# Kernel optimization log

Hardware: AMD Instinct MI355X
Metric: run time of the kernel (lower is better)

The kernel has to match this reference:

```python
import jax, jax.numpy as jnp
import numpy as np

B, N, HW, PS, FHW = 16, 4096, 224, 8, 56

def _gelu(x):
    return jax.nn.gelu(x, approximate=True)  # tanh approximation, matches nn.GELU(approximate='tanh')

def _conv(x, w, b, stride):
    y = jax.lax.conv_general_dilated(x, w, (stride, stride), [(1, 1), (1, 1)],
                                     dimension_numbers=('NCHW', 'OIHW', 'NCHW'))
    return y + b[None, :, None, None]

def _embed(points):
    # for i in 0..11: append sin(2^i * p) then cos(2^i * p) -> [B,N,48]
    factors = 2.0 ** jnp.arange(12, dtype=points.dtype)
    scaled = points[..., None, :] * factors[:, None]          # [B,N,12,2]
    feats = jnp.concatenate([jnp.sin(scaled), jnp.cos(scaled)], axis=-1)  # [B,N,12,4]
    return feats.reshape(points.shape[0], points.shape[1], 48)

def _extract_patches(fmap, points):
    # fmap [B,C,H,W]; points in [0,1]; bilinear grid_sample, zeros padding, align_corners=True
    Bq, C, H, W = fmap.shape
    centers = points * 2.0 - 1.0
    step = 2.0 / (W - 1)
    half = (PS - 1) / 2.0
    offs = jnp.linspace(-half, half, PS, dtype=fmap.dtype) * step
    offx2d, offy2d = jnp.meshgrid(offs, offs, indexing='ij')   # [ps,ps]
    gx = centers[..., 0][..., None, None] + offx2d             # [B,N,ps,ps]
    gy = centers[..., 1][..., None, None] + offy2d
    # align_corners=True pixel coords
    ix = (gx + 1.0) * 0.5 * (W - 1)
    iy = (gy + 1.0) * 0.5 * (H - 1)
    x0f = jnp.floor(ix); y0f = jnp.floor(iy)
    x0 = x0f.astype(jnp.int32); y0 = y0f.astype(jnp.int32)
    x1 = x0 + 1; y1 = y0 + 1
    wx1 = ix - x0f; wx0 = 1.0 - wx1
    wy1 = iy - y0f; wy0 = 1.0 - wy1
    fflat = fmap.reshape(Bq, C, H * W)

    def corner(xi, yi, w):
        valid = ((xi >= 0) & (xi < W) & (yi >= 0) & (yi < H)).astype(fmap.dtype)
        idx = jnp.clip(yi, 0, H - 1) * W + jnp.clip(xi, 0, W - 1)   # [B,N,ps,ps]
        vals = jax.vmap(lambda f, i: f[:, i])(fflat, idx)           # [B,C,N,ps,ps]
        return vals * (w * valid)[:, None]

    out = (corner(x0, y0, wx0 * wy0) + corner(x1, y0, wx1 * wy0)
           + corner(x0, y1, wx0 * wy1) + corner(x1, y1, wx1 * wy1))  # [B,C,N,ps,ps]
    return out.transpose(0, 2, 1, 3, 4)                              # [B,N,C,ps,ps]

def setup_inputs():
    key = jax.random.key(0)
    ks = jax.random.split(key, 26)
    def w(k, shape):
        fan_in = int(np.prod(shape[1:]))
        return jax.random.normal(k, shape, jnp.float32) * (1.0 / np.sqrt(fan_in))
    inp = {
        'points': jax.random.uniform(ks[0], (B, N, 2), jnp.float32),
        'images': jax.random.normal(ks[1], (B, 3, HW, HW), jnp.float32),
        # plane encoder
        'pw1': w(ks[2], (16, 3, 3, 3)),  'pb1': jnp.zeros((16,), jnp.float32),
        'pw2': w(ks[3], (32, 16, 3, 3)), 'pb2': jnp.zeros((32,), jnp.float32),
        'pw3': w(ks[4], (4, 32, 3, 3)),  'pb3': jnp.zeros((4,), jnp.float32),
        # global encoder
        'gw1': w(ks[5], (4, 3, 3, 3)),   'gb1': jnp.zeros((4,), jnp.float32),
        'gw2': w(ks[6], (8, 4, 3, 3)),   'gb2': jnp.zeros((8,), jnp.float32),
        'gw3': w(ks[7], (16, 8, 3, 3)),  'gb3': jnp.zeros((16,), jnp.float32),
        'gw4': w(ks[8], (32, 16, 3, 3)), 'gb4': jnp.zeros((32,), jnp.float32),
        'gw5': w(ks[9], (64, 32, 3, 3)), 'gb5': jnp.zeros((64,), jnp.float32),
        # point encoder (torch Linear: [out,in])
        'lw1': w(ks[10], (256, 48)),  'lb1': jnp.zeros((256,), jnp.float32),
        'lw2': w(ks[11], (256, 256)), 'lb2': jnp.zeros((256,), jnp.float32),
        # head
        'hw1': w(ks[12], (512, 576)), 'hb1': jnp.zeros((512,), jnp.float32),
        'hw2': w(ks[13], (1, 512)),   'hb2': jnp.zeros((1,), jnp.float32),
    }
    return inp

def reference(points, images, pw1, pb1, pw2, pb2, pw3, pb3,
              gw1, gb1, gw2, gb2, gw3, gb3, gw4, gb4, gw5, gb5,
              lw1, lb1, lw2, lb2, hw1, hb1, hw2, hb2):
    # point branch
    pe = _embed(points)                                         # [B,N,48]
    pf = _gelu(pe @ lw1.T + lb1) @ lw2.T + lb2                  # [B,N,256]
    # plane encoder -> 4x56x56 fmap
    f = _gelu(_conv(images, pw1, pb1, 2))
    f = _gelu(_conv(f, pw2, pb2, 2))
    fmap = _gelu(_conv(f, pw3, pb3, 1))                         # [B,4,56,56]
    # global encoder -> [B,64]
    g = images
    for wg, bg in ((gw1, gb1), (gw2, gb2), (gw3, gb3), (gw4, gb4), (gw5, gb5)):
        g = _gelu(_conv(g, wg, bg, 2))
    gc = g.mean(axis=(2, 3))                                    # AvgPool2d(7)+Flatten -> [B,64]
    gc = jnp.broadcast_to(gc[:, None, :], (points.shape[0], points.shape[1], 64))
    # per-point bilinear patch gather
    patches = _extract_patches(fmap, points).reshape(points.shape[0], points.shape[1], -1)  # [B,N,256]
    fused = jnp.concatenate([pf, patches, gc], axis=-1)         # [B,N,576]
    logit = _gelu(fused @ hw1.T + hb1) @ hw2.T + hb2            # [B,N,1]
    return logit
```

## Files before the change

### kernel.cpp

```cpp
#include <hip/hip_runtime.h>
#include <math.h>

#define BB 16
#define NN 4096
#define M_TOT (BB*NN)
#define TBK 32

typedef __attribute__((ext_vector_type(8))) short s8v;
typedef __attribute__((ext_vector_type(4))) float f4v;

__device__ __forceinline__ float gelu_t(float x){
    float u = 1.5957691216057308f * x * (1.0f + 0.044715f*x*x);
    return x / (1.0f + __expf(-u));
}

__device__ __forceinline__ unsigned short f2bf(float f){
    unsigned int u = __float_as_uint(f);
    u += 0x7fffu + ((u >> 16) & 1u);
    return (unsigned short)(u >> 16);
}

#define GLL(src, dst) __builtin_amdgcn_global_load_lds( \
    (const __attribute__((address_space(1))) void*)(src), \
    (__attribute__((address_space(3))) void*)(dst), 16, 0, 0)

template<int CIN, int COUT, int STRIDE, int CHUNK>
__device__ __forceinline__ void conv_dev2(
    const float* __restrict__ in, const float* __restrict__ w,
    const float* __restrict__ bias, float* __restrict__ out,
    int Hin, int Win, int Hout, int Wout, int bx, int by, int b, float* tile)
{
    constexpr int IW = 15*STRIDE + 3;
    constexpr int IH = IW;
    constexpr int PITCH = IW + 1;
    int tid = threadIdx.x;
    int tx = tid & 15, ty = tid >> 4;
    int wo = bx*16 + tx;
    int ho = by*16 + ty;
    int win0 = bx*16*STRIDE - 1;
    int hin0 = by*16*STRIDE - 1;
    bool valid = (wo < Wout) && (ho < Hout);

    float acc[COUT];
    #pragma unroll
    for (int co = 0; co < COUT; ++co) acc[co] = bias[co];

    const float* ib = in + (size_t)(b*CIN)*Hin*Win;
    for (int ci0 = 0; ci0 < CIN; ci0 += CHUNK) {
        __syncthreads();
        for (int idx = tid; idx < CHUNK*IH*IW; idx += 256) {
            int c = idx / (IH*IW), rem = idx - c*(IH*IW);
            int r = rem / IW, cc = rem - r*IW;
            int hi = hin0 + r, wi = win0 + cc;
            float v = 0.f;
            if ((unsigned)hi < (unsigned)Hin && (unsigned)wi < (unsigned)Win)
                v = ib[(size_t)(ci0 + c)*Hin*Win + hi*Win + wi];
            tile[c*IH*PITCH + r*PITCH + cc] = v;
        }
        __syncthreads();
        for (int ci = 0; ci < CHUNK; ++ci) {
            float vv[9];
            const float* tb = tile + ci*IH*PITCH;
            #pragma unroll
            for (int kh = 0; kh < 3; ++kh)
                #pragma unroll
                for (int kw = 0; kw < 3; ++kw)
                    vv[kh*3+kw] = tb[(ty*STRIDE + kh)*PITCH + tx*STRIDE + kw];
            const float* wc = w + (ci0 + ci)*9;
            #pragma unroll
            for (int co = 0; co < COUT; ++co) {
                const float* wp = wc + co*CIN*9;
                #pragma unroll
                for (int k = 0; k < 9; ++k)
                    acc[co] = fmaf(vv[k], wp[k], acc[co]);
            }
        }
    }
    if (valid) {
        size_t obase = ((size_t)b*COUT)*Hout*Wout + (size_t)ho*Wout + wo;
        #pragma unroll
        for (int co = 0; co < COUT; ++co)
            out[obase + (size_t)co*Hout*Wout] = gelu_t(acc[co]);
    }
}

__device__ __forceinline__ void conv_p3_dev(
    const float* __restrict__ in, const float* __restrict__ w,
    const float* __restrict__ bias, float4* __restrict__ out,
    int bx, int by, int b, float* tile)
{
    int tid = threadIdx.x;
    int tx = tid & 15, ty = tid >> 4;
    int wo = bx*16 + tx;
    int ho = by*16 + ty;
    int win0 = bx*16 - 1;
    int hin0 = by*16 - 1;
    bool valid = (ho < 56) && (wo < 56);

    const float* ib = in + (size_t)(b*32)*3136;
    __syncthreads();
    for (int idx = tid; idx < 32*324; idx += 256) {
        int c = idx / 324, rem = idx - c*324;
        int r = rem / 18, cc = rem - r*18;
        int hi = hin0 + r, wi = win0 + cc;
        float v = 0.f;
        if ((unsigned)hi < 56u && (unsigned)wi < 56u)
            v = ib[(size_t)c*3136 + hi*56 + wi];
        tile[c*342 + r*19 + cc] = v;
    }
    __syncthreads();
    float acc[4];
    #pragma unroll
    for (int co = 0; co < 4; ++co) acc[co] = bias[co];
    for (int ci = 0; ci < 32; ++ci) {
        float vv[9];
        const float* tb = tile + ci*342;
        #pragma unroll
        for (int kh = 0; kh < 3; ++kh)
            #pragma unroll
            for (int kw = 0; kw < 3; ++kw)
                vv[kh*3+kw] = tb[(ty + kh)*19 + tx + kw];
        #pragma unroll
        for (int co = 0; co < 4; ++co) {
            const float* wp = w + co*288 + ci*9;
            #pragma unroll
            for (int k = 0; k < 9; ++k)
                acc[co] = fmaf(vv[k], wp[k], acc[co]);
        }
    }
    if (valid) {
        float4 o;
        o.x = gelu_t(acc[0]); o.y = gelu_t(acc[1]);
        o.z = gelu_t(acc[2]); o.w = gelu_t(acc[3]);
        out[(size_t)b*3136 + (size_t)ho*56 + wo] = o;
    }
}

__global__ __launch_bounds__(256) void conv_dual_k(
    const float* __restrict__ in,
    const float* __restrict__ wA, const float* __restrict__ bA,
    const float* __restrict__ wB, const float* __restrict__ bB,
    float* __restrict__ outA, float* __restrict__ outB)
{
    __shared__ float tile[3*33*34];
    const int Hin = 224, Win = 224, Hout = 112, Wout = 112;
    int tid = threadIdx.x;
    int tx = tid & 15, ty = tid >> 4;
    int b = blockIdx.z;
    int wo = blockIdx.x*16 + tx;
    int ho = blockIdx.y*16 + ty;
    int win0 = blockIdx.x*32 - 1;
    int hin0 = blockIdx.y*32 - 1;

    const float* ib = in + (size_t)(b*3)*Hin*Win;
    for (int idx = tid; idx < 3*1089; idx += 256) {
        int c = idx / 1089, rem = idx - c*1089;
        int r = rem / 33, cc = rem - r*33;
        int hi = hin0 + r, wi = win0 + cc;
        float v = 0.f;
        if ((unsigned)hi < (unsigned)Hin && (unsigned)wi < (unsigned)Win)
            v = ib[(size_t)c*Hin*Win + hi*Win + wi];
        tile[c*33*34 + r*34 + cc] = v;
    }
    __syncthreads();

    float accA[16], accB[4];
    #pragma unroll
    for (int co = 0; co < 16; ++co) accA[co] = bA[co];
    #pragma unroll
    for (int co = 0; co < 4; ++co) accB[co] = bB[co];

    #pragma unroll
    for (int ci = 0; ci < 3; ++ci) {
        float vv[9];
        const float* tb = tile + ci*33*34;
        #pragma unroll
        for (int kh = 0; kh < 3; ++kh)
            #pragma unroll
            for (int kw = 0; kw < 3; ++kw)
                vv[kh*3+kw] = tb[(ty*2 + kh)*34 + tx*2 + kw];
        #pragma unroll
        for (int co = 0; co < 16; ++co) {
            const float* wp = wA + co*27 + ci*9;
            #pragma unroll
            for (int k = 0; k < 9; ++k) accA[co] = fmaf(vv[k], wp[k], accA[co]);
        }
        #pragma unroll
        for (int co = 0; co < 4; ++co) {
            const float* wp = wB + co*27 + ci*9;
            #pragma unroll
            for (int k = 0; k < 9; ++k) accB[co] = fmaf(vv[k], wp[k], accB[co]);
        }
    }
    size_t px = (size_t)ho*Wout + wo;
    #pragma unroll
    for (int co = 0; co < 16; ++co)
        outA[((size_t)(b*16 + co))*Hout*Wout + px] = gelu_t(accA[co]);
    #pragma unroll
    for (int co = 0; co < 4; ++co)
        outB[((size_t)(b*4 + co))*Hout*Wout + px] = gelu_t(accB[co]);
}

__global__ __launch_bounds__(256) void conv_pg2_k(
    const float* __restrict__ f1, const float* __restrict__ pw2, const float* __restrict__ pb2, float* __restrict__ f2,
    const float* __restrict__ g1, const float* __restrict__ gw2, const float* __restrict__ gb2, float* __restrict__ g2)
{
    __shared__ float tile[8*33*34];
    int z = blockIdx.z;
    if (z < 16) conv_dev2<16,32,2,8>(f1, pw2, pb2, f2, 112,112, 56,56, blockIdx.x, blockIdx.y, z, tile);
    else        conv_dev2<4,8,2,4> (g1, gw2, gb2, g2, 112,112, 56,56, blockIdx.x, blockIdx.y, z-16, tile);
}

__global__ __launch_bounds__(256) void conv_pg3_k(
    const float* __restrict__ f2, const float* __restrict__ pw3, const float* __restrict__ pb3, float4* __restrict__ fmap4,
    const float* __restrict__ g2, const float* __restrict__ gw3, const float* __restrict__ gb3, float* __restrict__ g3)
{
    __shared__ float tile[32*342];
    int z = blockIdx.z;
    if (z < 16) {
        conv_p3_dev(f2, pw3, pb3, fmap4, blockIdx.x, blockIdx.y, z, tile);
    } else {
        if (blockIdx.x >= 2 || blockIdx.y >= 2) return;
        conv_dev2<8,16,2,8>(g2, gw3, gb3, g3, 56,56, 28,28, blockIdx.x, blockIdx.y, z-16, tile);
    }
}

__global__ __launch_bounds__(256) void g4_k(
    const float* __restrict__ g3, const float* __restrict__ w4,
    const float* __restrict__ b4, float* __restrict__ g4)
{
    __shared__ float ws[32*144];
    int tid = threadIdx.x;
    for (int i = tid; i < 32*144; i += 256) ws[i] = w4[i];
    __syncthreads();
    int idx = blockIdx.x*256 + tid;
    if (idx >= 16*196) return;
    int b = idx / 196, px = idx - (idx/196)*196;
    int ho = px / 14, wo = px - (px/14)*14;
    const float* src = g3 + (size_t)b*16*784;
    float acc[32];
    #pragma unroll
    for (int co = 0; co < 32; ++co) acc[co] = b4[co];
    for (int ci = 0; ci < 16; ++ci) {
        #pragma unroll
        for (int kh = 0; kh < 3; ++kh) {
            int hi = ho*2 - 1 + kh;
            if ((unsigned)hi >= 28u) continue;
            #pragma unroll
            for (int kw = 0; kw < 3; ++kw) {
                int wi = wo*2 - 1 + kw;
                if ((unsigned)wi >= 28u) continue;
                float v = src[ci*784 + hi*28 + wi];
                int wofs = ci*9 + kh*3 + kw;
                #pragma unroll
                for (int co = 0; co < 32; ++co)
                    acc[co] = fmaf(v, ws[co*144 + wofs], acc[co]);
            }
        }
    }
    size_t obase = (size_t)b*32*196 + px;
    #pragma unroll
    for (int co = 0; co < 32; ++co)
        g4[obase + (size_t)co*196] = gelu_t(acc[co]);
}

__global__ __launch_bounds__(256) void g5_k(
    const float* __restrict__ g4, const float* __restrict__ w5,
    const float* __restrict__ b5, float* __restrict__ g5)
{
    __shared__ float ws[64*288];
    int tid = threadIdx.x;
    for (int i = tid; i < 64*288; i += 256) ws[i] = w5[i];
    __syncthreads();
    int idx = blockIdx.x*256 + tid;
    if (idx >= 16*49*2) return;
    int cg = idx & 1;
    int t = idx >> 1;
    int b = t / 49, px = t - (t/49)*49;
    int ho = px / 7, wo = px - (px/7)*7;
    const float* src = g4 + (size_t)b*32*196;
    const float* wsb = ws + cg*32*288;
    float acc[32];
    #pragma unroll
    for (int c = 0; c < 32; ++c) acc[c] = b5[cg*32 + c];
    for (int ci = 0; ci < 32; ++ci) {
        #pragma unroll
        for (int kh = 0; kh < 3; ++kh) {
            int hi = ho*2 - 1 + kh;
            if ((unsigned)hi >= 14u) continue;
            #pragma unroll
            for (int kw = 0; kw < 3; ++kw) {
                int wi = wo*2 - 1 + kw;
                if ((unsigned)wi >= 14u) continue;
                float v = src[ci*196 + hi*14 + wi];
                int wofs = ci*9 + kh*3 + kw;
                #pragma unroll
                for (int c = 0; c < 32; ++c)
                    acc[c] = fmaf(v, wsb[c*288 + wofs], acc[c]);
            }
        }
    }
    size_t obase = (size_t)b*64*49 + (size_t)cg*32*49 + px;
    #pragma unroll
    for (int c = 0; c < 32; ++c)
        g5[obase + (size_t)c*49] = gelu_t(acc[c]);
}

__global__ void avgpool7_k(const float* __restrict__ in, float* __restrict__ out){
    int i = blockIdx.x*blockDim.x + threadIdx.x;
    if (i >= BB*64) return;
    const float* p = in + (size_t)i*49;
    float s = 0.f;
    #pragma unroll
    for (int k = 0; k < 49; ++k) s += p[k];
    out[i] = s * (1.0f/49.0f);
}

__global__ void cvtall_k(const float* __restrict__ lw1, const float* __restrict__ lw2,
                         const float* __restrict__ hw1, unsigned short* __restrict__ blw1,
                         unsigned short* __restrict__ blw2, unsigned short* __restrict__ bhw1,
                         float* __restrict__ out, const float* __restrict__ b2){
    int i = blockIdx.x*blockDim.x + threadIdx.x;
    if (i < M_TOT) out[i] = b2[0];
    if (i < 256*64) {
        int r = i >> 6, c = i & 63;
        blw1[i] = (c < 48) ? f2bf(lw1[r*48 + c]) : 0;
        return;
    }
    int j = i - 256*64;
    if (j < 256*256) { blw2[j] = f2bf(lw2[j]); return; }
    j -= 256*256;
    if (j < 512*576) bhw1[j] = f2bf(hw1[j]);
}

__global__ __launch_bounds__(512) void mlp12_k(
    const float* __restrict__ points,
    const unsigned short* __restrict__ W1, const float* __restrict__ b1,
    const unsigned short* __restrict__ W2, const float* __restrict__ b2,
    unsigned short* __restrict__ C,
    const float4* __restrict__ fmap4, const float* __restrict__ gc)
{
    __shared__ unsigned short Hd[128*256];
    __shared__ unsigned short B2[256*TBK];
    int tid = threadIdx.x;
    int wv = tid >> 6, lane = tid & 63;
    int q = lane >> 4, lr = lane & 15;
    int mi = wv >> 2, ni = wv & 3;
    size_t m0 = (size_t)blockIdx.x * 128;

    f4v acc1[4][4];
    #pragma unroll
    for (int i = 0; i < 4; ++i)
        #pragma unroll
        for (int j = 0; j < 4; ++j) acc1[i][j] = (f4v){0.f,0.f,0.f,0.f};

    #pragma unroll
    for (int kb = 0; kb < 2; ++kb) {
        int seg = kb*4 + q;
        s8v a[4], b[4];
        #pragma unroll
        for (int t = 0; t < 4; ++t) {
            size_t m = m0 + mi*64 + t*16 + lr;
            float px = points[m*2], py = points[m*2+1];
            union { s8v v; unsigned short u[8]; } pk;
            #pragma unroll
            for (int j = 0; j < 8; ++j) {
                int k = seg*8 + j;
                unsigned short val = 0;
                if (k < 48) {
                    int i2 = k >> 2, rr = k & 3;
                    float f = (float)(1 << i2);
                    float p = (rr & 1) ? py : px;
                    float s = f * p;
                    val = f2bf((rr < 2) ? __sinf(s) : __cosf(s));
                }
                pk.u[j] = val;
            }
            a[t] = pk.v;
        }
        #pragma unroll
        for (int t = 0; t < 4; ++t) {
            int n = ni*64 + t*16 + lr;
            b[t] = *(const s8v*)(W1 + n*64 + seg*8);
        }
        #pragma unroll
        for (int mt = 0; mt < 4; ++mt)
            #pragma unroll
            for (int nt = 0; nt < 4; ++nt)
                acc1[mt][nt] = __builtin_amdgcn_mfma_f32_16x16x32_bf16(a[mt], b[nt], acc1[mt][nt], 0, 0, 0);
    }
    {
        float b1v[4];
        #pragma unroll
        for (int nt = 0; nt < 4; ++nt) b1v[nt] = b1[ni*64 + nt*16 + lr];
        #pragma unroll
        for (int mt = 0; mt < 4; ++mt)
            #pragma unroll
            for (int r4 = 0; r4 < 4; ++r4) {
                int row = mi*64 + mt*16 + q*4 + r4;
                #pragma unroll
                for (int nt = 0; nt < 4; ++nt) {
                    int col = ni*64 + nt*16 + lr;
                    float v = gelu_t(acc1[mt][nt][r4] + b1v[nt]);
                    int p = (col >> 3) ^ (row & 7);
                    Hd[(row*32 + p)*8 + (col & 7)] = f2bf(v);
                }
            }
    }
    __syncthreads();

    f4v acc2[4][4];
    #pragma unroll
    for (int i = 0; i < 4; ++i)
        #pragma unroll
        for (int j = 0; j < 4; ++j) acc2[i][j] = (f4v){0.f,0.f,0.f,0.f};

    for (int kt = 0; kt < 8; ++kt) {
        #pragma unroll
        for (int r = 0; r < 2; ++r) {
            int f = r*512 + tid;
            int rr = f >> 2, ll = (f & 3) ^ ((f >> 3) & 3);
            GLL(W2 + rr*256 + kt*32 + ll*8, B2 + f*8);
        }
        __syncthreads();
        s8v a[4], b[4];
        int sw = q ^ ((lr >> 1) & 3);
        #pragma unroll
        for (int t = 0; t < 4; ++t) {
            int row = mi*64 + t*16 + lr;
            int p = (kt*4 + q) ^ (row & 7);
            a[t] = *(const s8v*)(Hd + (row*32 + p)*8);
        }
        #pragma unroll
        for (int t = 0; t < 4; ++t) {
            int n = ni*64 + t*16 + lr;
            b[t] = *(const s8v*)(B2 + (n*4 + sw)*8);
        }
        #pragma unroll
        for (int mt = 0; mt < 4; ++mt)
            #pragma unroll
            for (int nt = 0; nt < 4; ++nt)
                acc2[mt][nt] = __builtin_amdgcn_mfma_f32_16x16x32_bf16(a[mt], b[nt], acc2[mt][nt], 0, 0, 0);
        __syncthreads();
    }
    {
        float b2v[4];
        #pragma unroll
        for (int nt = 0; nt < 4; ++nt) b2v[nt] = b2[ni*64 + nt*16 + lr];
        #pragma unroll
        for (int mt = 0; mt < 4; ++mt)
            #pragma unroll
            for (int r4 = 0; r4 < 4; ++r4) {
                size_t m = m0 + mi*64 + mt*16 + q*4 + r4;
                #pragma unroll
                for (int nt = 0; nt < 4; ++nt) {
                    int n = ni*64 + nt*16 + lr;
                    C[m*576 + n] = f2bf(acc2[mt][nt][r4] + b2v[nt]);
                }
            }
    }
    #pragma unroll 1
    for (int it = 0; it < 16; ++it) {
        int task = it*512 + tid;
        int ml = task >> 6, ij = task & 63;
        size_t m = m0 + ml;
        int i = ij >> 3, j = ij & 7;
        int b = (int)(m >> 12);
        float px = points[m*2], py = points[m*2+1];
        float cx = px*2.f - 1.f, cy = py*2.f - 1.f;
        const float step = 2.0f/55.0f;
        float gx = cx + ((float)i - 3.5f)*step;
        float gy = cy + ((float)j - 3.5f)*step;
        float ix = (gx + 1.f)*0.5f*55.f;
        float iy = (gy + 1.f)*0.5f*55.f;
        float x0f = floorf(ix), y0f = floorf(iy);
        int x0 = (int)x0f, y0 = (int)y0f;
        int x1 = x0 + 1,  y1 = y0 + 1;
        float wx1 = ix - x0f, wx0 = 1.f - wx1;
        float wy1 = iy - y0f, wy0 = 1.f - wy1;
        float v00 = ((x0>=0)&&(x0<56)&&(y0>=0)&&(y0<56)) ? 1.f : 0.f;
        float v10 = ((x1>=0)&&(x1<56)&&(y0>=0)&&(y0<56)) ? 1.f : 0.f;
        float v01 = ((x0>=0)&&(x0<56)&&(y1>=0)&&(y1<56)) ? 1.f : 0.f;
        float v11 = ((x1>=0)&&(x1<56)&&(y1>=0)&&(y1<56)) ? 1.f : 0.f;
        float w00 = wx0*wy0*v00, w10 = wx1*wy0*v10, w01 = wx0*wy1*v01, w11 = wx1*wy1*v11;
        int cx0 = min(max(x0,0),55), cx1 = min(max(x1,0),55);
        int cy0 = min(max(y0,0),55), cy1 = min(max(y1,0),55);
        const float4* fb = fmap4 + (size_t)b*3136;
        float4 f00 = fb[cy0*56 + cx0], f10 = fb[cy0*56 + cx1];
        float4 f01 = fb[cy1*56 + cx0], f11 = fb[cy1*56 + cx1];
        float4 v;
        v.x = w00*f00.x + w10*f10.x + w01*f01.x + w11*f11.x;
        v.y = w00*f00.y + w10*f10.y + w01*f01.y + w11*f11.y;
        v.z = w00*f00.z + w10*f10.z + w01*f01.z + w11*f11.z;
        v.w = w00*f00.w + w10*f10.w + w01*f01.w + w11*f11.w;
        C[m*576 + 256 +   0 + ij] = f2bf(v.x);
        C[m*576 + 256 +  64 + ij] = f2bf(v.y);
        C[m*576 + 256 + 128 + ij] = f2bf(v.z);
        C[m*576 + 256 + 192 + ij] = f2bf(v.w);
        C[m*576 + 512 + ij] = f2bf(gc[b*64 + ij]);
    }
}

__global__ __launch_bounds__(256, 3) void gemm_hd_k(
    const unsigned short* __restrict__ A,
    const unsigned short* __restrict__ W,
    const float* __restrict__ bias, const float* __restrict__ w2,
    float* __restrict__ out)
{
    __shared__ unsigned short As[64*TBK];
    __shared__ unsigned short Bs[256*TBK];
    __shared__ float red[4*64];
    int tid = threadIdx.x;
    int wv = tid >> 6, lane = tid & 63;
    int q = lane >> 4, lr = lane & 15;
    int sw = q ^ ((lr >> 1) & 3);
    int nq = wv * 64;
    size_t m0 = (size_t)blockIdx.x * 64;
    int nbase = blockIdx.y * 256;

    int rA = tid >> 2;
    int lA = (tid & 3) ^ ((tid >> 3) & 3);
    const unsigned short* srcA = A + (m0 + rA)*576 + lA*8;
    unsigned short* dstA = As + tid*8;
    const unsigned short* srcB[4]; unsigned short* dstB[4];
    #pragma unroll
    for (int r = 0; r < 4; ++r) {
        int f = r*256 + tid;
        int rr = f >> 2, ll = (f & 3) ^ ((f >> 3) & 3);
        srcB[r] = W + (size_t)(nbase + rr)*576 + ll*8;
        dstB[r] = Bs + f*8;
    }

    f4v acc[4][4];
    #pragma unroll
    for (int i = 0; i < 4; ++i)
        #pragma unroll
        for (int j = 0; j < 4; ++j) acc[i][j] = (f4v){0.f,0.f,0.f,0.f};

    for (int k0 = 0; k0 < 576; k0 += TBK) {
        GLL(srcA, dstA); srcA += TBK;
        #pragma unroll
        for (int r = 0; r < 4; ++r) { GLL(srcB[r], dstB[r]); srcB[r] += TBK; }
        __syncthreads();
        s8v a[4], b[4];
        #pragma unroll
        for (int t = 0; t < 4; ++t)
            a[t] = *(const s8v*)(As + (t*16 + lr)*TBK + sw*8);
        #pragma unroll
        for (int t = 0; t < 4; ++t)
            b[t] = *(const s8v*)(Bs + (nq + t*16 + lr)*TBK + sw*8);
        #pragma unroll
        for (int mt = 0; mt < 4; ++mt)
            #pragma unroll
            for (int nt = 0; nt < 4; ++nt)
                acc[mt][nt] = __builtin_amdgcn_mfma_f32_16x16x32_bf16(a[mt], b[nt], acc[mt][nt], 0, 0, 0);
        __syncthreads();
    }
    float bv[4], w2v[4];
    #pragma unroll
    for (int nt = 0; nt < 4; ++nt) {
        int n = nbase + nq + nt*16 + lr;
        bv[nt] = bias[n];
        w2v[nt] = w2[n];
    }
    #pragma unroll
    for (int mt = 0; mt < 4; ++mt)
        #pragma unroll
        for (int r4 = 0; r4 < 4; ++r4) {
            int ml = mt*16 + q*4 + r4;
            float s = 0.f;
            #pragma unroll
            for (int nt = 0; nt < 4; ++nt)
                s += gelu_t(acc[mt][nt][r4] + bv[nt]) * w2v[nt];
            #pragma unroll
            for (int off = 8; off > 0; off >>= 1) s += __shfl_down(s, off, 16);
            if (lr == 0) red[wv*64 + ml] = s;
        }
    __syncthreads();
    if (tid < 64) {
        float t = red[tid] + red[64 + tid] + red[128 + tid] + red[192 + tid];
        atomicAdd(&out[m0 + tid], t);
    }
}

extern "C" void kernel_launch(void* const* d_in, const int* in_sizes, int n_in,
                              void* d_out, int out_size, void* d_ws, size_t ws_size,
                              hipStream_t stream) {
    const float* points = (const float*)d_in[0];
    const float* images = (const float*)d_in[1];
    const float* pw1 = (const float*)d_in[2];  const float* pb1 = (const float*)d_in[3];
    const float* pw2 = (const float*)d_in[4];  const float* pb2 = (const float*)d_in[5];
    const float* pw3 = (const float*)d_in[6];  const float* pb3 = (const float*)d_in[7];
    const float* gw1 = (const float*)d_in[8];  const float* gb1 = (const float*)d_in[9];
    const float* gw2 = (const float*)d_in[10]; const float* gb2 = (const float*)d_in[11];
    const float* gw3 = (const float*)d_in[12]; const float* gb3 = (const float*)d_in[13];
    const float* gw4 = (const float*)d_in[14]; const float* gb4 = (const float*)d_in[15];
    const float* gw5 = (const float*)d_in[16]; const float* gb5 = (const float*)d_in[17];
    const float* lw1 = (const float*)d_in[18]; const float* lb1 = (const float*)d_in[19];
    const float* lw2 = (const float*)d_in[20]; const float* lb2 = (const float*)d_in[21];
    const float* hw1 = (const float*)d_in[22]; const float* hb1 = (const float*)d_in[23];
    const float* hw2 = (const float*)d_in[24]; const float* hb2 = (const float*)d_in[25];
    float* out = (float*)d_out;

    char* base = (char*)d_ws;
    unsigned short* fused_b = (unsigned short*)base;
    unsigned short* hid_b   = fused_b + (size_t)M_TOT*576;
    float4* fmap4 = (float4*)(hid_b + (size_t)M_TOT*256);
    float* gc   = (float*)(fmap4 + (size_t)16*3136);
    unsigned short* blw1 = (unsigned short*)(gc + 1024);
    unsigned short* blw2 = blw1 + 256*64;
    unsigned short* bhw1 = blw2 + 256*256;
    float* ct = (float*)base;
    float* f1 = ct;
    float* f2 = f1 + (size_t)16*16*112*112;
    float* g1 = f2 + (size_t)16*32*56*56;
    float* g2 = g1 + (size_t)16*4*112*112;
    float* g3 = g2 + (size_t)16*8*56*56;
    float* g4 = g3 + (size_t)16*16*28*28;
    float* g5 = g4 + (size_t)16*32*14*14;

    cvtall_k<<<1472, 256, 0, stream>>>(lw1, lw2, hw1, blw1, blw2, bhw1, out, hb2);
    conv_dual_k<<<dim3(7,7,16), 256, 0, stream>>>(images, pw1, pb1, gw1, gb1, f1, g1);
    conv_pg2_k<<<dim3(4,4,32), 256, 0, stream>>>(f1, pw2, pb2, f2, g1, gw2, gb2, g2);
    conv_pg3_k<<<dim3(4,4,32), 256, 0, stream>>>(f2, pw3, pb3, fmap4, g2, gw3, gb3, g3);
    g4_k<<<13, 256, 0, stream>>>(g3, gw4, gb4, g4);
    g5_k<<<7, 256, 0, stream>>>(g4, gw5, gb5, g5);
    avgpool7_k<<<4, 256, 0, stream>>>(g5, gc);
    mlp12_k<<<M_TOT/128, 512, 0, stream>>>(points, blw1, lb1, blw2, lb2, fused_b, fmap4, gc);
    gemm_hd_k<<<dim3(M_TOT/64, 2), 256, 0, stream>>>(fused_b, bhw1, hb1, hw2, out);
}
```

Baseline: 489.7 us.

## Widen parallelism of small global-encoder convs and fuse avgpool via atomics

Splits the plane conv2 over two output-channel halves to double block count, and rewrites the plane conv3 to read directly from global memory with one thread per pixel, dropping the large shared tile. The g4 and g5 convs now assign one output channel per thread with an NHWC intermediate, so they launch many more blocks. The avgpool kernel is removed: g5 atomically accumulates the pooled mean into gc, which cvtall zeroes first. The aim is to stop the tiny tail convs from running on a handful of blocks, at the cost of more redundant global loads and nondeterministic float summation order.

```diff
diff --git a/kernel.cpp b/kernel.cpp
--- a/kernel.cpp
+++ b/kernel.cpp
@@ -84,58 +84,6 @@
     }
 }
 
-__device__ __forceinline__ void conv_p3_dev(
-    const float* __restrict__ in, const float* __restrict__ w,
-    const float* __restrict__ bias, float4* __restrict__ out,
-    int bx, int by, int b, float* tile)
-{
-    int tid = threadIdx.x;
-    int tx = tid & 15, ty = tid >> 4;
-    int wo = bx*16 + tx;
-    int ho = by*16 + ty;
-    int win0 = bx*16 - 1;
-    int hin0 = by*16 - 1;
-    bool valid = (ho < 56) && (wo < 56);
-
-    const float* ib = in + (size_t)(b*32)*3136;
-    __syncthreads();
-    for (int idx = tid; idx < 32*324; idx += 256) {
-        int c = idx / 324, rem = idx - c*324;
-        int r = rem / 18, cc = rem - r*18;
-        int hi = hin0 + r, wi = win0 + cc;
-        float v = 0.f;
-        if ((unsigned)hi < 56u && (unsigned)wi < 56u)
-            v = ib[(size_t)c*3136 + hi*56 + wi];
-        tile[c*342 + r*19 + cc] = v;
-    }
-    __syncthreads();
-    float acc[4];
-    #pragma unroll
-    for (int co = 0; co < 4; ++co) acc[co] = bias[co];
-    for (int ci = 0; ci < 32; ++ci) {
-        float vv[9];
-        const float* tb = tile + ci*342;
-        #pragma unroll
-        for (int kh = 0; kh < 3; ++kh)
-            #pragma unroll
-            for (int kw = 0; kw < 3; ++kw)
-                vv[kh*3+kw] = tb[(ty + kh)*19 + tx + kw];
-        #pragma unroll
-        for (int co = 0; co < 4; ++co) {
-            const float* wp = w + co*288 + ci*9;
-            #pragma unroll
-            for (int k = 0; k < 9; ++k)
-                acc[co] = fmaf(vv[k], wp[k], acc[co]);
-        }
-    }
-    if (valid) {
-        float4 o;
-        o.x = gelu_t(acc[0]); o.y = gelu_t(acc[1]);
-        o.z = gelu_t(acc[2]); o.w = gelu_t(acc[3]);
-        out[(size_t)b*3136 + (size_t)ho*56 + wo] = o;
-    }
-}
-
 __global__ __launch_bounds__(256) void conv_dual_k(
     const float* __restrict__ in,
     const float* __restrict__ wA, const float* __restrict__ bA,
@@ -207,40 +155,72 @@
 {
     __shared__ float tile[8*33*34];
     int z = blockIdx.z;
-    if (z < 16) conv_dev2<16,32,2,8>(f1, pw2, pb2, f2, 112,112, 56,56, blockIdx.x, blockIdx.y, z, tile);
-    else        conv_dev2<4,8,2,4> (g1, gw2, gb2, g2, 112,112, 56,56, blockIdx.x, blockIdx.y, z-16, tile);
+    if (z < 32) {
+        int b = z >> 1, half = z & 1;
+        conv_dev2<16,16,2,8>(f1 + (size_t)b*16*12544, pw2 + half*2304, pb2 + half*16,
+                             f2 + ((size_t)(b*32 + half*16))*3136,
+                             112,112, 56,56, blockIdx.x, blockIdx.y, 0, tile);
+    } else {
+        conv_dev2<4,8,2,4>(g1, gw2, gb2, g2, 112,112, 56,56, blockIdx.x, blockIdx.y, z-32, tile);
+    }
 }
 
 __global__ __launch_bounds__(256) void conv_pg3_k(
     const float* __restrict__ f2, const float* __restrict__ pw3, const float* __restrict__ pb3, float4* __restrict__ fmap4,
     const float* __restrict__ g2, const float* __restrict__ gw3, const float* __restrict__ gb3, float* __restrict__ g3)
 {
-    __shared__ float tile[32*342];
+    __shared__ float tile[8*33*34];
     int z = blockIdx.z;
     if (z < 16) {
-        conv_p3_dev(f2, pw3, pb3, fmap4, blockIdx.x, blockIdx.y, z, tile);
+        int b = z;
+        int idx = blockIdx.x*256 + threadIdx.x;
+        if (idx >= 3136) return;
+        int ho = idx / 56, wo = idx - ho*56;
+        const float* ib = f2 + (size_t)b*32*3136;
+        float acc[4];
+        #pragma unroll
+        for (int co = 0; co < 4; ++co) acc[co] = pb3[co];
+        for (int ci = 0; ci < 32; ++ci) {
+            const float* ic = ib + (size_t)ci*3136;
+            #pragma unroll
+            for (int kh = 0; kh < 3; ++kh) {
+                int hi = ho - 1 + kh;
+                if ((unsigned)hi >= 56u) continue;
+                #pragma unroll
+                for (int kw = 0; kw < 3; ++kw) {
+                    int wi = wo - 1 + kw;
+                    if ((unsigned)wi >= 56u) continue;
+                    float v = ic[hi*56 + wi];
+                    int wofs = ci*9 + kh*3 + kw;
+                    #pragma unroll
+                    for (int co = 0; co < 4; ++co)
+                        acc[co] = fmaf(v, pw3[co*288 + wofs], acc[co]);
+                }
+            }
+        }
+        float4 o;
+        o.x = gelu_t(acc[0]); o.y = gelu_t(acc[1]);
+        o.z = gelu_t(acc[2]); o.w = gelu_t(acc[3]);
+        fmap4[(size_t)b*3136 + idx] = o;
     } else {
-        if (blockIdx.x >= 2 || blockIdx.y >= 2) return;
-        conv_dev2<8,16,2,8>(g2, gw3, gb3, g3, 56,56, 28,28, blockIdx.x, blockIdx.y, z-16, tile);
+        if (blockIdx.x >= 4) return;
+        int bx = blockIdx.x & 1, by = blockIdx.x >> 1;
+        conv_dev2<8,16,2,8>(g2, gw3, gb3, g3, 56,56, 28,28, bx, by, z-16, tile);
     }
 }
 
 __global__ __launch_bounds__(256) void g4_k(
     const float* __restrict__ g3, const float* __restrict__ w4,
-    const float* __restrict__ b4, float* __restrict__ g4)
-{
-    __shared__ float ws[32*144];
-    int tid = threadIdx.x;
-    for (int i = tid; i < 32*144; i += 256) ws[i] = w4[i];
-    __syncthreads();
-    int idx = blockIdx.x*256 + tid;
-    if (idx >= 16*196) return;
-    int b = idx / 196, px = idx - (idx/196)*196;
-    int ho = px / 14, wo = px - (px/14)*14;
+    const float* __restrict__ b4, float* __restrict__ g4o)
+{
+    int idx = blockIdx.x*256 + threadIdx.x;
+    int co = idx & 31;
+    int t = idx >> 5;
+    int b = t / 196, px = t - b*196;
+    int ho = px / 14, wo = px - ho*14;
     const float* src = g3 + (size_t)b*16*784;
-    float acc[32];
-    #pragma unroll
-    for (int co = 0; co < 32; ++co) acc[co] = b4[co];
+    const float* wp = w4 + co*144;
+    float acc = b4[co];
     for (int ci = 0; ci < 16; ++ci) {
         #pragma unroll
         for (int kh = 0; kh < 3; ++kh) {
@@ -250,39 +230,25 @@
             for (int kw = 0; kw < 3; ++kw) {
                 int wi = wo*2 - 1 + kw;
                 if ((unsigned)wi >= 28u) continue;
-                float v = src[ci*784 + hi*28 + wi];
-                int wofs = ci*9 + kh*3 + kw;
-                #pragma unroll
-                for (int co = 0; co < 32; ++co)
-                    acc[co] = fmaf(v, ws[co*144 + wofs], acc[co]);
-            }
-        }
-    }
-    size_t obase = (size_t)b*32*196 + px;
-    #pragma unroll
-    for (int co = 0; co < 32; ++co)
-        g4[obase + (size_t)co*196] = gelu_t(acc[co]);
+                acc = fmaf(src[ci*784 + hi*28 + wi], wp[ci*9 + kh*3 + kw], acc);
+            }
+        }
+    }
+    g4o[(size_t)b*6272 + px*32 + co] = gelu_t(acc);
 }
 
 __global__ __launch_bounds__(256) void g5_k(
-    const float* __restrict__ g4, const float* __restrict__ w5,
-    const float* __restrict__ b5, float* __restrict__ g5)
-{
-    __shared__ float ws[64*288];
-    int tid = threadIdx.x;
-    for (int i = tid; i < 64*288; i += 256) ws[i] = w5[i];
-    __syncthreads();
-    int idx = blockIdx.x*256 + tid;
-    if (idx >= 16*49*2) return;
-    int cg = idx & 1;
-    int t = idx >> 1;
-    int b = t / 49, px = t - (t/49)*49;
-    int ho = px / 7, wo = px - (px/7)*7;
-    const float* src = g4 + (size_t)b*32*196;
-    const float* wsb = ws + cg*32*288;
-    float acc[32];
-    #pragma unroll
-    for (int c = 0; c < 32; ++c) acc[c] = b5[cg*32 + c];
+    const float* __restrict__ g4o, const float* __restrict__ w5,
+    const float* __restrict__ b5, float* __restrict__ gc)
+{
+    int idx = blockIdx.x*256 + threadIdx.x;
+    int co = idx & 63;
+    int t = idx >> 6;
+    int b = t / 49, px = t - b*49;
+    int ho = px / 7, wo = px - ho*7;
+    const float* src = g4o + (size_t)b*6272;
+    const float* wp = w5 + co*288;
+    float acc = b5[co];
     for (int ci = 0; ci < 32; ++ci) {
         #pragma unroll
         for (int kh = 0; kh < 3; ++kh) {
@@ -292,36 +258,21 @@
             for (int kw = 0; kw < 3; ++kw) {
                 int wi = wo*2 - 1 + kw;
                 if ((unsigned)wi >= 14u) continue;
-                float v = src[ci*196 + hi*14 + wi];
-                int wofs = ci*9 + kh*3 + kw;
-                #pragma unroll
-                for (int c = 0; c < 32; ++c)
-                    acc[c] = fmaf(v, wsb[c*288 + wofs], acc[c]);
-            }
-        }
-    }
-    size_t obase = (size_t)b*64*49 + (size_t)cg*32*49 + px;
-    #pragma unroll
-    for (int c = 0; c < 32; ++c)
-        g5[obase + (size_t)c*49] = gelu_t(acc[c]);
-}
-
-__global__ void avgpool7_k(const float* __restrict__ in, float* __restrict__ out){
-    int i = blockIdx.x*blockDim.x + threadIdx.x;
-    if (i >= BB*64) return;
-    const float* p = in + (size_t)i*49;
-    float s = 0.f;
-    #pragma unroll
-    for (int k = 0; k < 49; ++k) s += p[k];
-    out[i] = s * (1.0f/49.0f);
+                acc = fmaf(src[(hi*14 + wi)*32 + ci], wp[ci*9 + kh*3 + kw], acc);
+            }
+        }
+    }
+    atomicAdd(&gc[b*64 + co], gelu_t(acc) * (1.0f/49.0f));
 }
 
 __global__ void cvtall_k(const float* __restrict__ lw1, const float* __restrict__ lw2,
                          const float* __restrict__ hw1, unsigned short* __restrict__ blw1,
                          unsigned short* __restrict__ blw2, unsigned short* __restrict__ bhw1,
-                         float* __restrict__ out, const float* __restrict__ b2){
+                         float* __restrict__ out, const float* __restrict__ b2,
+                         float* __restrict__ gc){
     int i = blockIdx.x*blockDim.x + threadIdx.x;
     if (i < M_TOT) out[i] = b2[0];
+    if (i < 1024) gc[i] = 0.f;
     if (i < 256*64) {
         int r = i >> 6, c = i & 63;
         blw1[i] = (c < 48) ? f2bf(lw1[r*48 + c]) : 0;
@@ -617,15 +568,13 @@
     float* g2 = g1 + (size_t)16*4*112*112;
     float* g3 = g2 + (size_t)16*8*56*56;
     float* g4 = g3 + (size_t)16*16*28*28;
-    float* g5 = g4 + (size_t)16*32*14*14;
-
-    cvtall_k<<<1472, 256, 0, stream>>>(lw1, lw2, hw1, blw1, blw2, bhw1, out, hb2);
+
+    cvtall_k<<<1472, 256, 0, stream>>>(lw1, lw2, hw1, blw1, blw2, bhw1, out, hb2, gc);
     conv_dual_k<<<dim3(7,7,16), 256, 0, stream>>>(images, pw1, pb1, gw1, gb1, f1, g1);
-    conv_pg2_k<<<dim3(4,4,32), 256, 0, stream>>>(f1, pw2, pb2, f2, g1, gw2, gb2, g2);
-    conv_pg3_k<<<dim3(4,4,32), 256, 0, stream>>>(f2, pw3, pb3, fmap4, g2, gw3, gb3, g3);
-    g4_k<<<13, 256, 0, stream>>>(g3, gw4, gb4, g4);
-    g5_k<<<7, 256, 0, stream>>>(g4, gw5, gb5, g5);
-    avgpool7_k<<<4, 256, 0, stream>>>(g5, gc);
+    conv_pg2_k<<<dim3(4,4,48), 256, 0, stream>>>(f1, pw2, pb2, f2, g1, gw2, gb2, g2);
+    conv_pg3_k<<<dim3(13,1,32), 256, 0, stream>>>(f2, pw3, pb3, fmap4, g2, gw3, gb3, g3);
+    g4_k<<<392, 256, 0, stream>>>(g3, gw4, gb4, g4);
+    g5_k<<<196, 256, 0, stream>>>(g4, gw5, gb5, gc);
     mlp12_k<<<M_TOT/128, 512, 0, stream>>>(points, blw1, lb1, blw2, lb2, fused_b, fmap4, gc);
     gemm_hd_k<<<dim3(M_TOT/64, 2), 256, 0, stream>>>(fused_b, bhw1, hb1, hw2, out);
 }
```

After: 433.3 us. -11.5%, faster.
